# Kernel optimization log

Measured on AMD Instinct MI355X. Metric: run time of the kernel, lower is better.

Reference implementation:

```python
import jax, jax.numpy as jnp
import numpy as np

B, T, N = 256, 512, 256
START, STOP = 254, 255


def setup_inputs() -> dict:
    key = jax.random.key(0)
    k1, k2, k3 = jax.random.split(key, 3)
    inputs = jax.random.normal(k1, (B, T, N), dtype=jnp.float32)
    transitions = jax.random.normal(k2, (N, N), dtype=jnp.float32)
    # sentinel rows/cols as in __init__
    transitions = transitions.at[START, :].set(-10000.0).at[:, STOP].set(-10000.0)
    tags = jax.random.randint(k3, (B, T), 0, N, dtype=jnp.int32)
    mask = jnp.ones((B, T), dtype=jnp.int32)
    return {"inputs": inputs, "transitions": transitions, "tags": tags, "mask": mask}


def _input_likelihood(inputs, transitions, fmask):
    # alpha[b, tag]: log-sum over paths ending at tag
    alpha0 = transitions[:, START][None, :] + inputs[:, 0, :]

    def step(alpha, xs):
        emit, m = xs  # emit: (B, N), m: (B,)
        # inner[b, next, prev] = alpha[b, prev] + (emit[b, next] + trans[next, prev]) * mask[b, i-1]
        inner = alpha[:, None, :] + (emit[:, :, None] + transitions[None, :, :]) * m[:, None, None]
        return jax.nn.logsumexp(inner, axis=-1), None

    xs = (jnp.swapaxes(inputs[:, 1:, :], 0, 1), jnp.swapaxes(fmask[:, :-1], 0, 1))
    alpha, _ = jax.lax.scan(step, alpha0, xs)
    stops = alpha + transitions[STOP][None, :]
    return jax.nn.logsumexp(stops, axis=-1)  # (B,)


def _joint_likelihood(inputs, transitions, tags, fmask):
    score = transitions[tags[:, 0], START]  # (B,)
    # transitions[next, prev] * mask[:, i+1], summed over steps
    trans_sc = transitions[tags[:, 1:], tags[:, :-1]] * fmask[:, 1:]
    # inputs[b, i, prev_tag] * mask[:, i]
    emit_sc = jnp.take_along_axis(inputs[:, :-1, :], tags[:, :-1, None], axis=2)[..., 0] * fmask[:, :-1]
    score = score + trans_sc.sum(axis=-1) + emit_sc.sum(axis=-1)
    last_idx = (fmask.sum(axis=-1) - 1.0).astype(jnp.int32)  # (B,)
    last_tags = jnp.take_along_axis(tags, last_idx[:, None], axis=1)[:, 0]
    last_input = jnp.take_along_axis(inputs[:, -1, :], last_tags[:, None], axis=1)[:, 0]
    return score + transitions[STOP, last_tags] + last_input * fmask[:, -1]


def reference(inputs, transitions, tags, mask):
    fmask = mask.astype(jnp.float32)
    log_denominator = _input_likelihood(inputs, transitions, fmask)
    log_numerator = _joint_likelihood(inputs, transitions, tags, fmask)
    return jnp.sum(log_numerator - log_denominator)
```

## Files before the change

### kernel.cpp

```cpp
#include <hip/hip_runtime.h>
#include <hip/hip_bf16.h>
#include <stdint.h>

#define B_    256
#define T_    512
#define N_    256
#define START_ 254
#define STOP_  255
#define GCOLS 16
#define NF    16
#define ND    32
#define LOG2E 1.4426950408889634f
#define LN2   0.6931471805599453f

#define WSB_OFF 65536
#define WCF_OFF 131072
#define WCB_OFF 131328
#define WNUM_OFF 131584

typedef __attribute__((ext_vector_type(4))) float floatx4;
typedef __attribute__((ext_vector_type(4))) unsigned int uintx4;
typedef __attribute__((ext_vector_type(8))) int v8i;

template<bool X> struct BC { static constexpr bool value = X; };

__device__ __forceinline__ void lds_barrier() {
    asm volatile("s_waitcnt lgkmcnt(0)\n\ts_barrier" ::: "memory");
}
__device__ __forceinline__ float fmax3(float a, float b, float c) {
    return fmaxf(fmaxf(a, b), c);
}

__device__ __forceinline__ int pk_fp8x4(float a, float b, float c, float d) {
    int r = __builtin_amdgcn_cvt_pk_fp8_f32(a, b, 0, false);
    return __builtin_amdgcn_cvt_pk_fp8_f32(c, d, r, true);
}
__device__ __forceinline__ int pk_bf8x4(float a, float b, float c, float d) {
    int r = __builtin_amdgcn_cvt_pk_bf8_f32(a, b, 0, false);
    return __builtin_amdgcn_cvt_pk_bf8_f32(c, d, r, true);
}

struct DenomShared {
    alignas(16) char  V[2][4096];
    alignas(16) float mbuf[GCOLS * 12];
    alignas(16) float sbuf[GCOLS * 20];
    int flag;
};

template<bool ISF>
__device__ __forceinline__ void denom_path(
    DenomShared& sh, const float* __restrict__ inputs,
    const float* __restrict__ trans, const int* __restrict__ mask,
    float* __restrict__ ws, int blkLocal)
{
    const int tid = threadIdx.x;
    const int w = tid >> 6;
    const int l = tid & 63;
    const int q = l >> 4;
    const int b = l & 15;
    const int bg = blkLocal * GCOLS + b;
    const int j0 = 32 * w + 4 * q;
    const int S = ISF ? 256 : 255;
    const int scl = 0x7F7F7F7F;

    auto EIDX = [](int s) { return ISF ? s : (511 - s); };
    auto MIDX = [](int s) { return ISF ? (s - 1) : (511 - s); };

    int wa[2];
    #pragma unroll
    for (int mt = 0; mt < 2; ++mt)
        wa[mt] = ((((2 * w + mt) >> 3) * 2 + mt) << 10)
               + ((w & 3) << 8) + (b << 4) + (q << 2);
    const int rbase = l << 4;

    v8i afrag[2][2];
    #pragma unroll
    for (int mt = 0; mt < 2; ++mt) {
        const int row = 32 * w + 16 * mt + b;
        #pragma unroll
        for (int c = 0; c < 2; ++c) {
            v8i a;
            #pragma unroll
            for (int g8 = 0; g8 < 8; ++g8) {
                float e[4];
                if (ISF) {
                    floatx4 t = *(const floatx4*)(trans + row * N_ + c * 128 + q * 32 + 4 * g8);
                    #pragma unroll
                    for (int ii = 0; ii < 4; ++ii)
                        e[ii] = __builtin_amdgcn_exp2f(t[ii] * LOG2E);
                } else {
                    #pragma unroll
                    for (int ii = 0; ii < 4; ++ii) {
                        const int k = c * 128 + q * 32 + 4 * g8 + ii;
                        e[ii] = __builtin_amdgcn_exp2f(trans[k * N_ + row] * LOG2E);
                    }
                }
                a[g8] = pk_fp8x4(e[0], e[1], e[2], e[3]);
            }
            afrag[mt][c] = a;
        }
    }

    {
        const int* mrow = mask + blkLocal * GCOLS * T_;
        bool hd = false;
        #pragma unroll
        for (int i = 0; i < GCOLS * T_ / 512; ++i)
            hd |= (mrow[tid + 512 * i] == 0);
        if (tid == 0) sh.flag = 0;
        __syncthreads();
        if (__any(hd) && l == 0) atomicOr(&sh.flag, 1);
        __syncthreads();
    }
    const bool anyDead = (sh.flag != 0);

    const float* emitp = inputs + (size_t)bg * T_ * N_;
    const int*   maskp = mask + bg * T_;
    int   Ci = 0;
    float u[2][4];

    if (ISF) {
        #pragma unroll
        for (int mt = 0; mt < 2; ++mt) {
            floatx4 em = *(const floatx4*)(emitp + j0 + 16 * mt);
            #pragma unroll
            for (int r = 0; r < 4; ++r) {
                const int j = j0 + 16 * mt + r;
                u[mt][r] = __builtin_amdgcn_exp2f((trans[j * N_ + START_] + em[r]) * LOG2E);
            }
        }
    } else {
        #pragma unroll
        for (int mt = 0; mt < 2; ++mt) {
            floatx4 st = *(const floatx4*)(trans + STOP_ * N_ + j0 + 16 * mt);
            #pragma unroll
            for (int r = 0; r < 4; ++r)
                u[mt][r] = __builtin_amdgcn_exp2f(st[r] * LOG2E);
        }
    }
    {
        float mx = fmaxf(fmax3(u[0][0], u[0][1], u[0][2]),
                         fmax3(u[0][3], u[1][0], fmax3(u[1][1], u[1][2], u[1][3])));
        float sm = 0.f;
        #pragma unroll
        for (int mt = 0; mt < 2; ++mt)
            #pragma unroll
            for (int r = 0; r < 4; ++r) sm += u[mt][r];
        mx = fmaxf(mx, __shfl_xor(mx, 16, 64));
        mx = fmaxf(mx, __shfl_xor(mx, 32, 64));
        if (l < 16) sh.mbuf[b * 12 + w] = mx;
        sm += __shfl_xor(sm, 32, 64);
        if (l < 32) sh.sbuf[b * 20 + w * 2 + q] = sm;

        float xpi[2][4] = {{1.f,1.f,1.f,1.f},{1.f,1.f,1.f,1.f}};
        if (!ISF) {
            #pragma unroll
            for (int mt = 0; mt < 2; ++mt) {
                floatx4 e = *(const floatx4*)(emitp + (size_t)511 * N_ + j0 + 16 * mt);
                #pragma unroll
                for (int r = 0; r < 4; ++r)
                    xpi[mt][r] = __builtin_amdgcn_exp2f(e[r] * LOG2E);
            }
        }
        #pragma unroll
        for (int mt = 0; mt < 2; ++mt)
            *(int*)(sh.V[0] + wa[mt]) =
                pk_bf8x4(u[mt][0] * xpi[mt][0], u[mt][1] * xpi[mt][1],
                         u[mt][2] * xpi[mt][2], u[mt][3] * xpi[mt][3]);
    }

    auto run = [&](auto fastc) {
        constexpr bool FAST = decltype(fastc)::value;
        const long estep = ISF ? (long)N_ : -(long)N_;
        const int  mstep = ISF ? 1 : -1;

        floatx4 xc0, xc1;
        floatx4 rbA0, rbA1;
        floatx4 rbB0, rbB1;
        const float* pe = emitp + (size_t)EIDX(1) * N_ + j0;
        {
            floatx4 e0 = *(const floatx4*)pe;
            floatx4 e1 = *(const floatx4*)(pe + 16);
            pe += estep;
            rbA0 = *(const floatx4*)pe;
            rbA1 = *(const floatx4*)(pe + 16);
            pe += estep;
            rbB0 = *(const floatx4*)pe;
            rbB1 = *(const floatx4*)(pe + 16);
            pe += estep;
            #pragma unroll
            for (int r = 0; r < 4; ++r) {
                xc0[r] = __builtin_amdgcn_exp2f(e0[r] * LOG2E);
                xc1[r] = __builtin_amdgcn_exp2f(e1[r] * LOG2E);
            }
        }
        float mrot[2] = {1.f, 1.f};
        const int* pm = maskp;
        if (!FAST) {
            mrot[0] = (float)maskp[MIDX(1)];
            mrot[1] = (float)maskp[MIDX(2)];
            pm = maskp + MIDX(3);
        }
        lds_barrier();

        auto body = [&](int pr, int cur) {
            const char* vb = sh.V[pr];
            uintx4 r00 = *(const uintx4*)(vb + rbase);
            uintx4 r01 = *(const uintx4*)(vb + 1024 + rbase);
            uintx4 r10 = *(const uintx4*)(vb + 2048 + rbase);
            uintx4 r11 = *(const uintx4*)(vb + 3072 + rbase);
            const float* mb = &sh.mbuf[b * 12];
            floatx4 m0 = *(const floatx4*)mb;
            floatx4 m1 = *(const floatx4*)(mb + 4);
            floatx4 eC0 = *(const floatx4*)pe;
            floatx4 eC1 = *(const floatx4*)(pe + 16);
            float mC = 1.f;
            if (!FAST) mC = (float)(*pm);

            floatx4 xn0, xn1;
            #pragma unroll
            for (int r = 0; r < 4; ++r) {
                xn0[r] = __builtin_amdgcn_exp2f(rbA0[r] * LOG2E);
                xn1[r] = __builtin_amdgcn_exp2f(rbA1[r] * LOG2E);
            }

            floatx4 mv;
            #pragma unroll
            for (int r = 0; r < 4; ++r) mv[r] = fmaxf(m0[r], m1[r]);
            const float cmax = fmax3(mv[0], mv[1], fmaxf(mv[2], mv[3]));
            const uint32_t cb = __builtin_bit_cast(uint32_t, cmax);
            const int eb = (int)((cb >> 23) & 0xFFu);
            const float rs = __builtin_bit_cast(float, (uint32_t)(249 - eb) << 23);
            Ci += eb;

            floatx4 rx0, rx1;
            if (ISF) {
                #pragma unroll
                for (int r = 0; r < 4; ++r) { rx0[r] = xc0[r] * rs; rx1[r] = xc1[r] * rs; }
            }

            union { v8i v; struct { uintx4 lo, hi; } p; } bf0, bf1;
            bf0.p.lo = r00; bf0.p.hi = r01;
            bf1.p.lo = r10; bf1.p.hi = r11;

            floatx4 a0 = {0.f,0.f,0.f,0.f}, a1 = {0.f,0.f,0.f,0.f};
            a0 = __builtin_amdgcn_mfma_scale_f32_16x16x128_f8f6f4(
                     afrag[0][0], bf0.v, a0, 0, 1, 0, scl, 0, scl);
            a1 = __builtin_amdgcn_mfma_scale_f32_16x16x128_f8f6f4(
                     afrag[1][0], bf0.v, a1, 0, 1, 0, scl, 0, scl);
            a0 = __builtin_amdgcn_mfma_scale_f32_16x16x128_f8f6f4(
                     afrag[0][1], bf1.v, a0, 0, 1, 0, scl, 0, scl);
            a1 = __builtin_amdgcn_mfma_scale_f32_16x16x128_f8f6f4(
                     afrag[1][1], bf1.v, a1, 0, 1, 0, scl, 0, scl);

            if (FAST) {
                #pragma unroll
                for (int r = 0; r < 4; ++r) {
                    if (ISF) {
                        u[0][r] = a0[r] * rx0[r];
                        u[1][r] = a1[r] * rx1[r];
                    } else {
                        u[0][r] = a0[r] * rs;
                        u[1][r] = a1[r] * rs;
                    }
                }
            } else {
                const bool live = (mrot[cur] != 0.f);
                float csv = 0.f;
                if (__any(!live)) {
                    const float* sb = &sh.sbuf[b * 20];
                    floatx4 s0 = *(const floatx4*)sb,       s1 = *(const floatx4*)(sb + 4);
                    floatx4 s2 = *(const floatx4*)(sb + 8), s3 = *(const floatx4*)(sb + 12);
                    csv = ((((s0[0] + s0[1]) + (s0[2] + s0[3])) +
                            ((s1[0] + s1[1]) + (s1[2] + s1[3]))) +
                           (((s2[0] + s2[1]) + (s2[2] + s2[3])) +
                            ((s3[0] + s3[1]) + (s3[2] + s3[3])))) * rs;
                }
                #pragma unroll
                for (int r = 0; r < 4; ++r) {
                    if (ISF) {
                        u[0][r] = live ? a0[r] * rx0[r] : csv;
                        u[1][r] = live ? a1[r] * rx1[r] : csv;
                    } else {
                        u[0][r] = live ? a0[r] * rs : csv;
                        u[1][r] = live ? a1[r] * rs : csv;
                    }
                }
            }

            {
                float mx = fmaxf(fmax3(u[0][0], u[0][1], u[0][2]),
                                 fmax3(u[0][3], u[1][0],
                                       fmax3(u[1][1], u[1][2], u[1][3])));
                mx = fmaxf(mx, __shfl_xor(mx, 16, 64));
                mx = fmaxf(mx, __shfl_xor(mx, 32, 64));
                if (l < 16) sh.mbuf[b * 12 + w] = mx;
                if (!FAST) {
                    float sm = ((u[0][0] + u[0][1]) + (u[0][2] + u[0][3]))
                             + ((u[1][0] + u[1][1]) + (u[1][2] + u[1][3]));
                    sm += __shfl_xor(sm, 32, 64);
                    if (l < 32) sh.sbuf[b * 20 + w * 2 + q] = sm;
                }
            }
            if (ISF) {
                *(int*)(sh.V[pr ^ 1] + wa[0]) = pk_bf8x4(u[0][0], u[0][1], u[0][2], u[0][3]);
                *(int*)(sh.V[pr ^ 1] + wa[1]) = pk_bf8x4(u[1][0], u[1][1], u[1][2], u[1][3]);
            } else {
                *(int*)(sh.V[pr ^ 1] + wa[0]) =
                    pk_bf8x4(u[0][0] * xc0[0], u[0][1] * xc0[1],
                             u[0][2] * xc0[2], u[0][3] * xc0[3]);
                *(int*)(sh.V[pr ^ 1] + wa[1]) =
                    pk_bf8x4(u[1][0] * xc1[0], u[1][1] * xc1[1],
                             u[1][2] * xc1[2], u[1][3] * xc1[3]);
            }
            lds_barrier();
            xc0 = xn0; xc1 = xn1;
            rbA0 = rbB0; rbA1 = rbB1;
            rbB0 = eC0;  rbB1 = eC1;
            pe += estep;
            if (!FAST) { mrot[cur] = mC; pm += mstep; }
        };

        #pragma unroll 1
        for (int g = 0; g < S / 2; ++g) {
            body(0, 0);
            body(1, 1);
        }
        if (S & 1) body(0, 0);
    };

    if (anyDead) run(BC<false>{});
    else         run(BC<true>{});

    float* wsV = ws + (ISF ? 0 : WSB_OFF);
    #pragma unroll
    for (int mt = 0; mt < 2; ++mt) {
        floatx4 vv = {u[mt][0], u[mt][1], u[mt][2], u[mt][3]};
        *(floatx4*)&wsV[(size_t)bg * N_ + j0 + 16 * mt] = vv;
    }
    if (tid < 16) {
        float* wsC = ws + (ISF ? WCF_OFF : WCB_OFF);
        wsC[blkLocal * GCOLS + tid] = (float)(Ci - 122 * S);
    }
}

__global__ __launch_bounds__(512, 2) void crf_main(
    const float* __restrict__ inputs, const float* __restrict__ trans,
    const int* __restrict__ tags, const int* __restrict__ mask,
    float* __restrict__ out, float* __restrict__ ws)
{
    __shared__ DenomShared sh;

    if (blockIdx.x >= ND) {
        float* nred = sh.sbuf;
        int*   nredi = (int*)(sh.sbuf + 8);
        const int bb = blockIdx.x - ND;
        const int t  = threadIdx.x;
        const int tg = tags[bb * T_ + t];
        const float fm = (float)mask[bb * T_ + t];
        float part = 0.f;
        if (t >= 1)      part += trans[tg * N_ + tags[bb * T_ + t - 1]] * fm;
        if (t <= T_ - 2) part += inputs[((size_t)bb * T_ + t) * N_ + tg] * fm;
        int ms = mask[bb * T_ + t];
        #pragma unroll
        for (int off = 1; off < 64; off <<= 1) {
            part += __shfl_xor(part, off, 64);
            ms   += __shfl_xor(ms, off, 64);
        }
        if ((t & 63) == 0) { nred[t >> 6] = part; nredi[t >> 6] = ms; }
        __syncthreads();
        if (t == 0) {
            float tot = 0.f; int mtot = 0;
            for (int i = 0; i < 8; ++i) { tot += nred[i]; mtot += nredi[i]; }
            tot += trans[tags[bb * T_] * N_ + START_];
            const int last = mtot - 1;
            const int lt = tags[bb * T_ + last];
            tot += trans[STOP_ * N_ + lt]
                 + inputs[((size_t)bb * T_ + (T_ - 1)) * N_ + lt]
                   * (float)mask[bb * T_ + T_ - 1];
            ws[WNUM_OFF + bb] = tot;
        }
        return;
    }

    if (blockIdx.x < NF) denom_path<true>(sh, inputs, trans, mask, ws, blockIdx.x);
    else                 denom_path<false>(sh, inputs, trans, mask, ws, blockIdx.x - NF);
}

__global__ __launch_bounds__(256) void crf_combine(
    const float* __restrict__ ws, float* __restrict__ out)
{
    __shared__ float red[4];
    const int t = threadIdx.x;
    const int w = t >> 6, l = t & 63;
    float acc = 0.f;
    #pragma unroll 1
    for (int i = 0; i < 4; ++i) {
        const int bb = blockIdx.x * GCOLS + w * 4 + i;
        const float* pa = ws + (size_t)bb * N_;
        const float* pb = ws + WSB_OFF + (size_t)bb * N_;
        floatx4 va = *(const floatx4*)(pa + 4 * l);
        floatx4 vb = *(const floatx4*)(pb + 4 * l);
        float p = va[0] * vb[0] + va[1] * vb[1] + va[2] * vb[2] + va[3] * vb[3];
        #pragma unroll
        for (int off = 1; off < 64; off <<= 1) p += __shfl_xor(p, off, 64);
        if (l == 0) {
            const float denom = (ws[WCF_OFF + bb] + ws[WCB_OFF + bb]
                                 + __builtin_amdgcn_logf(p)) * LN2;
            acc += ws[WNUM_OFF + bb] - denom;
        }
    }
    if (l == 0) red[w] = acc;
    __syncthreads();
    if (t == 0) atomicAdd(out, red[0] + red[1] + red[2] + red[3]);
}

extern "C" void kernel_launch(void* const* d_in, const int* in_sizes, int n_in,
                              void* d_out, int out_size, void* d_ws, size_t ws_size,
                              hipStream_t stream) {
    const float* inputs = (const float*)d_in[0];
    const float* trans  = (const float*)d_in[1];
    const int*   tags   = (const int*)d_in[2];
    const int*   mask   = (const int*)d_in[3];
    float* out = (float*)d_out;
    float* ws  = (float*)d_ws;
    hipMemsetAsync(out, 0, sizeof(float), stream);
    crf_main<<<dim3(ND + B_), dim3(512), 0, stream>>>(inputs, trans, tags, mask, out, ws);
    crf_combine<<<dim3(B_ / GCOLS), dim3(256), 0, stream>>>(ws, out);
}
```

Measured before the change: 338.1 us.

## Halve denominator block to 4 waves with 64 rows each, use permlane swaps

Each denominator block now uses 256 threads (4 waves), and each wave covers 64 output rows with four MFMA tiles instead of two. This halves the number of waves meeting at the per-step LDS barrier and shrinks the cross-wave max buffer. Cross-lane max and sum reductions switch from __shfl_xor to v_permlane16/32_swap. Emission prefetching is restructured into a 2-slot ring indexed by step parity. The tradeoff is twice the per-wave MFMA and exp work on the serial recurrence and higher register pressure. The numerator blocks are adapted so each thread handles two timesteps.

```diff
diff --git a/kernel.cpp b/kernel.cpp
--- a/kernel.cpp
+++ b/kernel.cpp
@@ -30,6 +30,21 @@
 __device__ __forceinline__ float fmax3(float a, float b, float c) {
     return fmaxf(fmaxf(a, b), c);
 }
+__device__ __forceinline__ float pmax16(float x) {
+    float a = x, b = x;
+    asm("v_permlane16_swap_b32 %0, %1" : "+v"(a), "+v"(b));
+    return fmaxf(a, b);
+}
+__device__ __forceinline__ float pmax32(float x) {
+    float a = x, b = x;
+    asm("v_permlane32_swap_b32 %0, %1" : "+v"(a), "+v"(b));
+    return fmaxf(a, b);
+}
+__device__ __forceinline__ float psum32(float x) {
+    float a = x, b = x;
+    asm("v_permlane32_swap_b32 %0, %1" : "+v"(a), "+v"(b));
+    return a + b;
+}
 
 __device__ __forceinline__ int pk_fp8x4(float a, float b, float c, float d) {
     int r = __builtin_amdgcn_cvt_pk_fp8_f32(a, b, 0, false);
@@ -42,7 +57,7 @@
 
 struct DenomShared {
     alignas(16) char  V[2][4096];
-    alignas(16) float mbuf[GCOLS * 12];
+    alignas(16) float mbuf[GCOLS * 4];
     alignas(16) float sbuf[GCOLS * 20];
     int flag;
 };
@@ -59,24 +74,28 @@
     const int q = l >> 4;
     const int b = l & 15;
     const int bg = blkLocal * GCOLS + b;
-    const int j0 = 32 * w + 4 * q;
+    const int j0 = 64 * w + 4 * q;
     const int S = ISF ? 256 : 255;
     const int scl = 0x7F7F7F7F;
 
     auto EIDX = [](int s) { return ISF ? s : (511 - s); };
     auto MIDX = [](int s) { return ISF ? (s - 1) : (511 - s); };
 
-    int wa[2];
+    int wa[4];
     #pragma unroll
-    for (int mt = 0; mt < 2; ++mt)
-        wa[mt] = ((((2 * w + mt) >> 3) * 2 + mt) << 10)
-               + ((w & 3) << 8) + (b << 4) + (q << 2);
+    for (int mt = 0; mt < 4; ++mt) {
+        const int idx  = 4 * w + mt;
+        const int cc   = idx >> 3;
+        const int rbit = idx & 1;
+        const int qk   = (idx >> 1) & 3;
+        wa[mt] = ((cc * 2 + rbit) << 10) + (qk << 8) + (b << 4) + (q << 2);
+    }
     const int rbase = l << 4;
 
-    v8i afrag[2][2];
+    v8i afrag[4][2];
     #pragma unroll
-    for (int mt = 0; mt < 2; ++mt) {
-        const int row = 32 * w + 16 * mt + b;
+    for (int mt = 0; mt < 4; ++mt) {
+        const int row = 64 * w + 16 * mt + b;
         #pragma unroll
         for (int c = 0; c < 2; ++c) {
             v8i a;
@@ -105,8 +124,8 @@
         const int* mrow = mask + blkLocal * GCOLS * T_;
         bool hd = false;
         #pragma unroll
-        for (int i = 0; i < GCOLS * T_ / 512; ++i)
-            hd |= (mrow[tid + 512 * i] == 0);
+        for (int i = 0; i < GCOLS * T_ / 256; ++i)
+            hd |= (mrow[tid + 256 * i] == 0);
         if (tid == 0) sh.flag = 0;
         __syncthreads();
         if (__any(hd) && l == 0) atomicOr(&sh.flag, 1);
@@ -117,11 +136,11 @@
     const float* emitp = inputs + (size_t)bg * T_ * N_;
     const int*   maskp = mask + bg * T_;
     int   Ci = 0;
-    float u[2][4];
+    float u[4][4];
 
     if (ISF) {
         #pragma unroll
-        for (int mt = 0; mt < 2; ++mt) {
+        for (int mt = 0; mt < 4; ++mt) {
             floatx4 em = *(const floatx4*)(emitp + j0 + 16 * mt);
             #pragma unroll
             for (int r = 0; r < 4; ++r) {
@@ -131,7 +150,7 @@
         }
     } else {
         #pragma unroll
-        for (int mt = 0; mt < 2; ++mt) {
+        for (int mt = 0; mt < 4; ++mt) {
             floatx4 st = *(const floatx4*)(trans + STOP_ * N_ + j0 + 16 * mt);
             #pragma unroll
             for (int r = 0; r < 4; ++r)
@@ -139,23 +158,25 @@
         }
     }
     {
-        float mx = fmaxf(fmax3(u[0][0], u[0][1], u[0][2]),
-                         fmax3(u[0][3], u[1][0], fmax3(u[1][1], u[1][2], u[1][3])));
-        float sm = 0.f;
-        #pragma unroll
-        for (int mt = 0; mt < 2; ++mt)
-            #pragma unroll
-            for (int r = 0; r < 4; ++r) sm += u[mt][r];
-        mx = fmaxf(mx, __shfl_xor(mx, 16, 64));
-        mx = fmaxf(mx, __shfl_xor(mx, 32, 64));
-        if (l < 16) sh.mbuf[b * 12 + w] = mx;
-        sm += __shfl_xor(sm, 32, 64);
+        float mx = u[0][0], sm = 0.f;
+        #pragma unroll
+        for (int mt = 0; mt < 4; ++mt)
+            #pragma unroll
+            for (int r = 0; r < 4; ++r) { mx = fmaxf(mx, u[mt][r]); sm += u[mt][r]; }
+        mx = pmax16(mx);
+        mx = pmax32(mx);
+        if (l < 16) sh.mbuf[b * 4 + w] = mx;
+        sm = psum32(sm);
         if (l < 32) sh.sbuf[b * 20 + w * 2 + q] = sm;
 
-        float xpi[2][4] = {{1.f,1.f,1.f,1.f},{1.f,1.f,1.f,1.f}};
+        float xpi[4][4];
+        #pragma unroll
+        for (int mt = 0; mt < 4; ++mt)
+            #pragma unroll
+            for (int r = 0; r < 4; ++r) xpi[mt][r] = 1.f;
         if (!ISF) {
             #pragma unroll
-            for (int mt = 0; mt < 2; ++mt) {
+            for (int mt = 0; mt < 4; ++mt) {
                 floatx4 e = *(const floatx4*)(emitp + (size_t)511 * N_ + j0 + 16 * mt);
                 #pragma unroll
                 for (int r = 0; r < 4; ++r)
@@ -163,7 +184,7 @@
             }
         }
         #pragma unroll
-        for (int mt = 0; mt < 2; ++mt)
+        for (int mt = 0; mt < 4; ++mt)
             *(int*)(sh.V[0] + wa[mt]) =
                 pk_bf8x4(u[mt][0] * xpi[mt][0], u[mt][1] * xpi[mt][1],
                          u[mt][2] * xpi[mt][2], u[mt][3] * xpi[mt][3]);
@@ -174,25 +195,25 @@
         const long estep = ISF ? (long)N_ : -(long)N_;
         const int  mstep = ISF ? 1 : -1;
 
-        floatx4 xc0, xc1;
-        floatx4 rbA0, rbA1;
-        floatx4 rbB0, rbB1;
+        floatx4 xc[4];
+        floatx4 rb[2][4];
         const float* pe = emitp + (size_t)EIDX(1) * N_ + j0;
         {
-            floatx4 e0 = *(const floatx4*)pe;
-            floatx4 e1 = *(const floatx4*)(pe + 16);
+            floatx4 e1[4];
+            #pragma unroll
+            for (int mt = 0; mt < 4; ++mt) e1[mt] = *(const floatx4*)(pe + 16 * mt);
             pe += estep;
-            rbA0 = *(const floatx4*)pe;
-            rbA1 = *(const floatx4*)(pe + 16);
+            #pragma unroll
+            for (int mt = 0; mt < 4; ++mt) rb[0][mt] = *(const floatx4*)(pe + 16 * mt);
             pe += estep;
-            rbB0 = *(const floatx4*)pe;
-            rbB1 = *(const floatx4*)(pe + 16);
+            #pragma unroll
+            for (int mt = 0; mt < 4; ++mt) rb[1][mt] = *(const floatx4*)(pe + 16 * mt);
             pe += estep;
             #pragma unroll
-            for (int r = 0; r < 4; ++r) {
-                xc0[r] = __builtin_amdgcn_exp2f(e0[r] * LOG2E);
-                xc1[r] = __builtin_amdgcn_exp2f(e1[r] * LOG2E);
-            }
+            for (int mt = 0; mt < 4; ++mt)
+                #pragma unroll
+                for (int r = 0; r < 4; ++r)
+                    xc[mt][r] = __builtin_amdgcn_exp2f(e1[mt][r] * LOG2E);
         }
         float mrot[2] = {1.f, 1.f};
         const int* pm = maskp;
@@ -209,115 +230,105 @@
             uintx4 r01 = *(const uintx4*)(vb + 1024 + rbase);
             uintx4 r10 = *(const uintx4*)(vb + 2048 + rbase);
             uintx4 r11 = *(const uintx4*)(vb + 3072 + rbase);
-            const float* mb = &sh.mbuf[b * 12];
+            const float* mb = &sh.mbuf[b * 4];
             floatx4 m0 = *(const floatx4*)mb;
-            floatx4 m1 = *(const floatx4*)(mb + 4);
-            floatx4 eC0 = *(const floatx4*)pe;
-            floatx4 eC1 = *(const floatx4*)(pe + 16);
             float mC = 1.f;
             if (!FAST) mC = (float)(*pm);
 
-            floatx4 xn0, xn1;
-            #pragma unroll
-            for (int r = 0; r < 4; ++r) {
-                xn0[r] = __builtin_amdgcn_exp2f(rbA0[r] * LOG2E);
-                xn1[r] = __builtin_amdgcn_exp2f(rbA1[r] * LOG2E);
-            }
-
-            floatx4 mv;
-            #pragma unroll
-            for (int r = 0; r < 4; ++r) mv[r] = fmaxf(m0[r], m1[r]);
-            const float cmax = fmax3(mv[0], mv[1], fmaxf(mv[2], mv[3]));
+            floatx4 xn[4];
+            #pragma unroll
+            for (int mt = 0; mt < 4; ++mt)
+                #pragma unroll
+                for (int r = 0; r < 4; ++r)
+                    xn[mt][r] = __builtin_amdgcn_exp2f(rb[cur][mt][r] * LOG2E);
+            #pragma unroll
+            for (int mt = 0; mt < 4; ++mt)
+                rb[cur][mt] = *(const floatx4*)(pe + 16 * mt);
+            pe += estep;
+
+            const float cmax = fmax3(m0[0], m0[1], fmaxf(m0[2], m0[3]));
             const uint32_t cb = __builtin_bit_cast(uint32_t, cmax);
             const int eb = (int)((cb >> 23) & 0xFFu);
             const float rs = __builtin_bit_cast(float, (uint32_t)(249 - eb) << 23);
             Ci += eb;
 
-            floatx4 rx0, rx1;
+            floatx4 rx[4];
             if (ISF) {
                 #pragma unroll
-                for (int r = 0; r < 4; ++r) { rx0[r] = xc0[r] * rs; rx1[r] = xc1[r] * rs; }
+                for (int mt = 0; mt < 4; ++mt)
+                    #pragma unroll
+                    for (int r = 0; r < 4; ++r) rx[mt][r] = xc[mt][r] * rs;
             }
 
             union { v8i v; struct { uintx4 lo, hi; } p; } bf0, bf1;
             bf0.p.lo = r00; bf0.p.hi = r01;
             bf1.p.lo = r10; bf1.p.hi = r11;
 
-            floatx4 a0 = {0.f,0.f,0.f,0.f}, a1 = {0.f,0.f,0.f,0.f};
-            a0 = __builtin_amdgcn_mfma_scale_f32_16x16x128_f8f6f4(
-                     afrag[0][0], bf0.v, a0, 0, 1, 0, scl, 0, scl);
-            a1 = __builtin_amdgcn_mfma_scale_f32_16x16x128_f8f6f4(
-                     afrag[1][0], bf0.v, a1, 0, 1, 0, scl, 0, scl);
-            a0 = __builtin_amdgcn_mfma_scale_f32_16x16x128_f8f6f4(
-                     afrag[0][1], bf1.v, a0, 0, 1, 0, scl, 0, scl);
-            a1 = __builtin_amdgcn_mfma_scale_f32_16x16x128_f8f6f4(
-                     afrag[1][1], bf1.v, a1, 0, 1, 0, scl, 0, scl);
+            floatx4 acc[4];
+            #pragma unroll
+            for (int mt = 0; mt < 4; ++mt) {
+                floatx4 z = {0.f, 0.f, 0.f, 0.f};
+                z = __builtin_amdgcn_mfma_scale_f32_16x16x128_f8f6f4(
+                        afrag[mt][0], bf0.v, z, 0, 1, 0, scl, 0, scl);
+                acc[mt] = __builtin_amdgcn_mfma_scale_f32_16x16x128_f8f6f4(
+                        afrag[mt][1], bf1.v, z, 0, 1, 0, scl, 0, scl);
+            }
 
             if (FAST) {
                 #pragma unroll
-                for (int r = 0; r < 4; ++r) {
-                    if (ISF) {
-                        u[0][r] = a0[r] * rx0[r];
-                        u[1][r] = a1[r] * rx1[r];
-                    } else {
-                        u[0][r] = a0[r] * rs;
-                        u[1][r] = a1[r] * rs;
-                    }
-                }
+                for (int mt = 0; mt < 4; ++mt)
+                    #pragma unroll
+                    for (int r = 0; r < 4; ++r)
+                        u[mt][r] = ISF ? acc[mt][r] * rx[mt][r] : acc[mt][r] * rs;
             } else {
                 const bool live = (mrot[cur] != 0.f);
                 float csv = 0.f;
                 if (__any(!live)) {
                     const float* sb = &sh.sbuf[b * 20];
-                    floatx4 s0 = *(const floatx4*)sb,       s1 = *(const floatx4*)(sb + 4);
-                    floatx4 s2 = *(const floatx4*)(sb + 8), s3 = *(const floatx4*)(sb + 12);
-                    csv = ((((s0[0] + s0[1]) + (s0[2] + s0[3])) +
-                            ((s1[0] + s1[1]) + (s1[2] + s1[3]))) +
-                           (((s2[0] + s2[1]) + (s2[2] + s2[3])) +
-                            ((s3[0] + s3[1]) + (s3[2] + s3[3])))) * rs;
+                    floatx4 s0 = *(const floatx4*)sb, s1 = *(const floatx4*)(sb + 4);
+                    csv = (((s0[0] + s0[1]) + (s0[2] + s0[3])) +
+                           ((s1[0] + s1[1]) + (s1[2] + s1[3]))) * rs;
                 }
                 #pragma unroll
-                for (int r = 0; r < 4; ++r) {
-                    if (ISF) {
-                        u[0][r] = live ? a0[r] * rx0[r] : csv;
-                        u[1][r] = live ? a1[r] * rx1[r] : csv;
-                    } else {
-                        u[0][r] = live ? a0[r] * rs : csv;
-                        u[1][r] = live ? a1[r] * rs : csv;
+                for (int mt = 0; mt < 4; ++mt)
+                    #pragma unroll
+                    for (int r = 0; r < 4; ++r) {
+                        const float lv = ISF ? acc[mt][r] * rx[mt][r] : acc[mt][r] * rs;
+                        u[mt][r] = live ? lv : csv;
                     }
-                }
             }
 
             {
-                float mx = fmaxf(fmax3(u[0][0], u[0][1], u[0][2]),
-                                 fmax3(u[0][3], u[1][0],
-                                       fmax3(u[1][1], u[1][2], u[1][3])));
-                mx = fmaxf(mx, __shfl_xor(mx, 16, 64));
-                mx = fmaxf(mx, __shfl_xor(mx, 32, 64));
-                if (l < 16) sh.mbuf[b * 12 + w] = mx;
+                float t0 = fmax3(u[0][0], u[0][1], u[0][2]);
+                t0 = fmax3(t0, u[0][3], u[1][0]);
+                t0 = fmax3(t0, u[1][1], u[1][2]);
+                t0 = fmax3(t0, u[1][3], u[2][0]);
+                t0 = fmax3(t0, u[2][1], u[2][2]);
+                t0 = fmax3(t0, u[2][3], u[3][0]);
+                t0 = fmax3(t0, u[3][1], u[3][2]);
+                t0 = fmaxf(t0, u[3][3]);
+                t0 = pmax16(t0);
+                t0 = pmax32(t0);
+                if (l < 16) sh.mbuf[b * 4 + w] = t0;
                 if (!FAST) {
-                    float sm = ((u[0][0] + u[0][1]) + (u[0][2] + u[0][3]))
-                             + ((u[1][0] + u[1][1]) + (u[1][2] + u[1][3]));
-                    sm += __shfl_xor(sm, 32, 64);
+                    float sm = (((u[0][0] + u[0][1]) + (u[0][2] + u[0][3])) +
+                                ((u[1][0] + u[1][1]) + (u[1][2] + u[1][3]))) +
+                               (((u[2][0] + u[2][1]) + (u[2][2] + u[2][3])) +
+                                ((u[3][0] + u[3][1]) + (u[3][2] + u[3][3])));
+                    sm = psum32(sm);
                     if (l < 32) sh.sbuf[b * 20 + w * 2 + q] = sm;
                 }
             }
-            if (ISF) {
-                *(int*)(sh.V[pr ^ 1] + wa[0]) = pk_bf8x4(u[0][0], u[0][1], u[0][2], u[0][3]);
-                *(int*)(sh.V[pr ^ 1] + wa[1]) = pk_bf8x4(u[1][0], u[1][1], u[1][2], u[1][3]);
-            } else {
-                *(int*)(sh.V[pr ^ 1] + wa[0]) =
-                    pk_bf8x4(u[0][0] * xc0[0], u[0][1] * xc0[1],
-                             u[0][2] * xc0[2], u[0][3] * xc0[3]);
-                *(int*)(sh.V[pr ^ 1] + wa[1]) =
-                    pk_bf8x4(u[1][0] * xc1[0], u[1][1] * xc1[1],
-                             u[1][2] * xc1[2], u[1][3] * xc1[3]);
+            #pragma unroll
+            for (int mt = 0; mt < 4; ++mt) {
+                *(int*)(sh.V[pr ^ 1] + wa[mt]) = ISF
+                    ? pk_bf8x4(u[mt][0], u[mt][1], u[mt][2], u[mt][3])
+                    : pk_bf8x4(u[mt][0] * xc[mt][0], u[mt][1] * xc[mt][1],
+                               u[mt][2] * xc[mt][2], u[mt][3] * xc[mt][3]);
             }
             lds_barrier();
-            xc0 = xn0; xc1 = xn1;
-            rbA0 = rbB0; rbA1 = rbB1;
-            rbB0 = eC0;  rbB1 = eC1;
-            pe += estep;
+            #pragma unroll
+            for (int mt = 0; mt < 4; ++mt) xc[mt] = xn[mt];
             if (!FAST) { mrot[cur] = mC; pm += mstep; }
         };
 
@@ -334,7 +345,7 @@
 
     float* wsV = ws + (ISF ? 0 : WSB_OFF);
     #pragma unroll
-    for (int mt = 0; mt < 2; ++mt) {
+    for (int mt = 0; mt < 4; ++mt) {
         floatx4 vv = {u[mt][0], u[mt][1], u[mt][2], u[mt][3]};
         *(floatx4*)&wsV[(size_t)bg * N_ + j0 + 16 * mt] = vv;
     }
@@ -344,7 +355,7 @@
     }
 }
 
-__global__ __launch_bounds__(512, 2) void crf_main(
+__global__ __launch_bounds__(256, 1) void crf_main(
     const float* __restrict__ inputs, const float* __restrict__ trans,
     const int* __restrict__ tags, const int* __restrict__ mask,
     float* __restrict__ out, float* __restrict__ ws)
@@ -356,12 +367,17 @@
         int*   nredi = (int*)(sh.sbuf + 8);
         const int bb = blockIdx.x - ND;
         const int t  = threadIdx.x;
-        const int tg = tags[bb * T_ + t];
-        const float fm = (float)mask[bb * T_ + t];
         float part = 0.f;
-        if (t >= 1)      part += trans[tg * N_ + tags[bb * T_ + t - 1]] * fm;
-        if (t <= T_ - 2) part += inputs[((size_t)bb * T_ + t) * N_ + tg] * fm;
-        int ms = mask[bb * T_ + t];
+        int   ms = 0;
+        #pragma unroll
+        for (int h = 0; h < 2; ++h) {
+            const int tt = t + 256 * h;
+            const int tg = tags[bb * T_ + tt];
+            const float fm = (float)mask[bb * T_ + tt];
+            if (tt >= 1)      part += trans[tg * N_ + tags[bb * T_ + tt - 1]] * fm;
+            if (tt <= T_ - 2) part += inputs[((size_t)bb * T_ + tt) * N_ + tg] * fm;
+            ms += mask[bb * T_ + tt];
+        }
         #pragma unroll
         for (int off = 1; off < 64; off <<= 1) {
             part += __shfl_xor(part, off, 64);
@@ -371,7 +387,7 @@
         __syncthreads();
         if (t == 0) {
             float tot = 0.f; int mtot = 0;
-            for (int i = 0; i < 8; ++i) { tot += nred[i]; mtot += nredi[i]; }
+            for (int i = 0; i < 4; ++i) { tot += nred[i]; mtot += nredi[i]; }
             tot += trans[tags[bb * T_] * N_ + START_];
             const int last = mtot - 1;
             const int lt = tags[bb * T_ + last];
@@ -425,6 +441,6 @@
     float* out = (float*)d_out;
     float* ws  = (float*)d_ws;
     hipMemsetAsync(out, 0, sizeof(float), stream);
-    crf_main<<<dim3(ND + B_), dim3(512), 0, stream>>>(inputs, trans, tags, mask, out, ws);
+    crf_main<<<dim3(ND + B_), dim3(256), 0, stream>>>(inputs, trans, tags, mask, out, ws);
     crf_combine<<<dim3(B_ / GCOLS), dim3(256), 0, stream>>>(ws, out);
 }
```

After: 358.2 us. +6.0%, slower.
